# Kernel tuning notes

Measured on AMD Instinct MI355X. Metric: run time of the kernel, lower is better.

## Reference

```python
import jax, jax.numpy as jnp
import numpy as np

BATCH = 2
TIME_N = 196
SPACE_F = 8
D_MODEL = 768
N_HEADS = 12
D_STATE = 16
DT_RANK = 48  # ceil(768/16)
D_CONV = 4
SEQ = 1 + TIME_N * SPACE_F


def _ln(x, w, b, eps=1e-5):
    m = x.mean(-1, keepdims=True)
    v = ((x - m) ** 2).mean(-1, keepdims=True)
    return (x - m) * jax.lax.rsqrt(v + eps) * w + b


def _silu(x):
    return x * jax.nn.sigmoid(x)


def _causal_conv(x, w, b):
    # x: (B, L, d); depthwise causal conv1d, kernel D_CONV, padding left
    L = x.shape[1]
    xp = jnp.pad(x, ((0, 0), (D_CONV - 1, 0), (0, 0)))
    return sum(xp[:, k:k + L, :] * w[:, k] for k in range(D_CONV)) + b


def _ssm(u, delta, A, Bm, C, Dp):
    # u, delta: (B,L,d); A: (d,N); Bm, C: (B,L,N)
    dA = jnp.exp(delta[..., None] * A)                    # (B,L,d,N)
    dBu = (delta * u)[..., None] * Bm[:, :, None, :]      # (B,L,d,N)
    B, L, d, N = dA.shape

    def step(h, inp):
        a, bu = inp
        h = a * h + bu
        return h, h

    _, hs = jax.lax.scan(step, jnp.zeros((B, d, N), dA.dtype),
                         (dA.transpose(1, 0, 2, 3), dBu.transpose(1, 0, 2, 3)))
    return jnp.einsum('lbdn,bln->bld', hs, C) + u * Dp


def _mamba_dir(xp, z, conv_w, conv_b, xproj_w, dt_w, dt_b, A_log, Dp, flip):
    if flip:
        xp = xp[:, ::-1]
        z = z[:, ::-1]
    xc = _silu(_causal_conv(xp, conv_w, conv_b))
    x_dbl = xc @ xproj_w.T
    dt = x_dbl[..., :DT_RANK]
    Bm = x_dbl[..., DT_RANK:DT_RANK + D_STATE]
    C = x_dbl[..., DT_RANK + D_STATE:]
    delta = jax.nn.softplus(dt @ dt_w.T + dt_b)
    y = _ssm(xc, delta, -jnp.exp(A_log), Bm, C, Dp) * _silu(z)
    if flip:
        y = y[:, ::-1]
    return y


def _mamba(x, in_w, cw, cb, xw, dw, db, Al, Dp, cwb, cbb, xwb, dwb, dbb, Alb, Dpb, out_w):
    # bimamba v2: forward scan + backward (flipped) scan, summed, then out_proj
    xz = x @ in_w.T
    xp, z = jnp.split(xz, 2, axis=-1)
    y = (_mamba_dir(xp, z, cw, cb, xw, dw, db, Al, Dp, False)
         + _mamba_dir(xp, z, cwb, cbb, xwb, dwb, dbb, Alb, Dpb, True))
    return y @ out_w.T


def _mha(x, in_w, in_b, out_w, out_b):
    # torch nn.MultiheadAttention default (batch_first=False):
    # x is (L, N, E); attention runs over dim 0 (L), dim 1 (N) is batch.
    L, N, E = x.shape
    hd = E // N_HEADS
    qkv = x @ in_w.T + in_b
    q, k, v = jnp.split(qkv, 3, axis=-1)
    q = q.reshape(L, N, N_HEADS, hd)
    k = k.reshape(L, N, N_HEADS, hd)
    v = v.reshape(L, N, N_HEADS, hd)
    scores = jnp.einsum('lnhk,mnhk->nhlm', q, k) / jnp.sqrt(jnp.asarray(hd, x.dtype))
    o = jnp.einsum('nhlm,mnhk->lnhk', jax.nn.softmax(scores, axis=-1), v)
    return o.reshape(L, N, E) @ out_w.T + out_b


def _forward(x, norm1_w, norm1_b, norm2_w, norm2_b, norm3_w, norm3_b,
             attn_in_w, attn_in_b, attn_out_w, attn_out_b,
             m_in_w, m_conv_w, m_conv_b, m_xproj_w, m_dt_w, m_dt_b, m_Alog, m_D,
             m_conv_wb, m_conv_bb, m_xproj_wb, m_dt_wb, m_dt_bb, m_Alog_b, m_D_b,
             m_out_w, fc1_w, fc1_b, fc2_w, fc2_b, time_n, space_f):
    b, _, d = x.shape
    init_cls = x[:, :1]
    res_x = x
    # 'b (n t) d -> (b n) t d'
    xt = x[:, 1:].reshape(b, time_n, space_f, d).reshape(b * time_n, space_f, d)
    time_out = _mamba(_ln(xt, norm3_w, norm3_b), m_in_w, m_conv_w, m_conv_b,
                      m_xproj_w, m_dt_w, m_dt_b, m_Alog, m_D,
                      m_conv_wb, m_conv_bb, m_xproj_wb, m_dt_wb, m_dt_bb,
                      m_Alog_b, m_D_b, m_out_w)
    time_res = (xt + time_out).reshape(b, time_n, space_f, d)
    # cls repeat: 'b t d -> (b t) 1 d'
    cls = jnp.repeat(init_cls, space_f, axis=1).reshape(b * space_f, 1, d)
    # 'b (n t) d -> (b t) n d'
    xs = time_res.transpose(0, 2, 1, 3).reshape(b * space_f, time_n, d)
    xs = jnp.concatenate([cls, xs], axis=1)  # (b*t, n+1, d)
    space_out = _mha(_ln(xs, norm1_w, norm1_b), attn_in_w, attn_in_b, attn_out_w, attn_out_b)
    cls_tok = space_out[:, 0].reshape(b, space_f, d).mean(1, keepdims=True)
    # '(b t) n d -> b (n t) d'
    sp = space_out[:, 1:].reshape(b, space_f, time_n, d).transpose(0, 2, 1, 3).reshape(b, time_n * space_f, d)
    x = res_x + jnp.concatenate([cls_tok, sp], axis=1)
    h = _ln(x, norm2_w, norm2_b)
    h = jax.nn.gelu(h @ fc1_w.T + fc1_b, approximate=False) @ fc2_w.T + fc2_b
    return x + h


def setup_inputs():
    ks = iter(jax.random.split(jax.random.key(0), 64))

    def nrm(shape, s=0.02):
        return jax.random.normal(next(ks), shape, dtype=jnp.float32) * s

    d = D_MODEL
    Alog = jnp.log(jnp.tile(jnp.arange(1, D_STATE + 1, dtype=jnp.float32), (d, 1)))
    return dict(
        x=jax.random.normal(next(ks), (BATCH, SEQ, d), dtype=jnp.float32),
        norm1_w=jnp.ones((d,), jnp.float32), norm1_b=jnp.zeros((d,), jnp.float32),
        norm2_w=jnp.ones((d,), jnp.float32), norm2_b=jnp.zeros((d,), jnp.float32),
        norm3_w=jnp.ones((d,), jnp.float32), norm3_b=jnp.zeros((d,), jnp.float32),
        attn_in_w=nrm((3 * d, d)), attn_in_b=nrm((3 * d,)),
        attn_out_w=nrm((d, d)), attn_out_b=nrm((d,)),
        m_in_w=nrm((2 * d, d)),
        m_conv_w=nrm((d, D_CONV), 0.2), m_conv_b=nrm((d,), 0.1),
        m_xproj_w=nrm((DT_RANK + 2 * D_STATE, d)),
        m_dt_w=nrm((d, DT_RANK), 0.1), m_dt_b=nrm((d,), 0.5),
        m_Alog=Alog, m_D=jnp.ones((d,), jnp.float32),
        m_conv_wb=nrm((d, D_CONV), 0.2), m_conv_bb=nrm((d,), 0.1),
        m_xproj_wb=nrm((DT_RANK + 2 * D_STATE, d)),
        m_dt_wb=nrm((d, DT_RANK), 0.1), m_dt_bb=nrm((d,), 0.5),
        m_Alog_b=Alog, m_D_b=jnp.ones((d,), jnp.float32),
        m_out_w=nrm((d, d)),
        fc1_w=nrm((4 * d, d)), fc1_b=nrm((4 * d,), 0.01),
        fc2_w=nrm((d, 4 * d)), fc2_b=nrm((d,), 0.01),
        time_n=TIME_N, space_f=SPACE_F,
    )


def reference(x, norm1_w, norm1_b, norm2_w, norm2_b, norm3_w, norm3_b,
              attn_in_w, attn_in_b, attn_out_w, attn_out_b,
              m_in_w, m_conv_w, m_conv_b, m_xproj_w, m_dt_w, m_dt_b, m_Alog, m_D,
              m_conv_wb, m_conv_bb, m_xproj_wb, m_dt_wb, m_dt_bb, m_Alog_b, m_D_b,
              m_out_w, fc1_w, fc1_b, fc2_w, fc2_b, time_n, space_f):
    return _forward(x, norm1_w, norm1_b, norm2_w, norm2_b, norm3_w, norm3_b,
                    attn_in_w, attn_in_b, attn_out_w, attn_out_b,
                    m_in_w, m_conv_w, m_conv_b, m_xproj_w, m_dt_w, m_dt_b, m_Alog, m_D,
                    m_conv_wb, m_conv_bb, m_xproj_wb, m_dt_wb, m_dt_bb, m_Alog_b, m_D_b,
                    m_out_w, fc1_w, fc1_b, fc2_w, fc2_b, time_n, space_f)
```

## Files before the change

kernel.cpp:

```cpp
#include <hip/hip_runtime.h>
#include <hip/hip_bf16.h>
#include <math.h>

#define DM 768
#define NBATCH 2
#define TIMEN 196
#define SPACEF 8
#define SEQL 1569
#define NSTATE 16
#define MT 3136
#define NSEQ 392
#define AT 3152
#define XTOK 3138

typedef __attribute__((ext_vector_type(8))) short s16x8;
typedef __attribute__((ext_vector_type(4))) float f32x4;
typedef __hip_bfloat16 bf16;

__device__ __forceinline__ float silu_fast(float x){ return __fdividef(x, 1.0f + __expf(-x)); }
__device__ __forceinline__ float geluf(float x){ return 0.5f*x*(1.0f + erff(x*0.70710678118654752f)); }
__device__ __forceinline__ float softplusf(float x){ return (x > 20.0f) ? x : log1pf(expf(x)); }
__device__ __forceinline__ int imin(int a, int b){ return a < b ? a : b; }

#define GLD_LDS16(g, l) __builtin_amdgcn_global_load_lds( \
    (const __attribute__((address_space(1))) void*)(g), \
    (__attribute__((address_space(3))) void*)(l), 16, 0, 0)

template<int N, int K, int Np, int Kp>
__device__ __forceinline__ void cvt_seg(const float* __restrict__ src, bf16* __restrict__ dst){
  const int total = Np * Kp;
  int base = blockIdx.x * 1024 + threadIdx.x;
  #pragma unroll
  for (int e = 0; e < 4; e++){
    int idx = base + e * 256;
    if (idx < total){
      int n = idx / Kp, k = idx % Kp;
      float v = (n < N && k < K) ? src[n * K + k] : 0.0f;
      dst[idx] = __float2bfloat16(v);
    }
  }
}

__global__ __launch_bounds__(256) void cvtw_kernel(
    const float* s0, const float* s1, const float* s2, const float* s3,
    const float* s4, const float* s5, const float* s6, const float* s7,
    const float* s8, const float* s9, bf16* w)
{
  switch (blockIdx.y) {
    case 0: cvt_seg<1536,768,1536,768>(s0, w + 0);        break;
    case 1: cvt_seg<  80,768, 128,768>(s1, w + 1179648);  break;
    case 2: cvt_seg<  80,768, 128,768>(s2, w + 1277952);  break;
    case 3: cvt_seg< 768, 48, 768, 64>(s3, w + 1376256);  break;
    case 4: cvt_seg< 768, 48, 768, 64>(s4, w + 1425408);  break;
    case 5: cvt_seg< 768,768, 768,768>(s5, w + 1474560);  break;
    case 6: cvt_seg<2304,768,2304,768>(s6, w + 2064384);  break;
    case 7: cvt_seg< 768,768, 768,768>(s7, w + 3833856);  break;
    case 8: cvt_seg<3072,768,3072,768>(s8, w + 4423680);  break;
    default:cvt_seg< 768,3072,768,3072>(s9, w + 6782976); break;
  }
}

__device__ __forceinline__ float block_sum256(float v, float* sm){
  #pragma unroll
  for (int o = 32; o > 0; o >>= 1) v += __shfl_down(v, o);
  __syncthreads();
  if ((threadIdx.x & 63) == 0) sm[threadIdx.x >> 6] = v;
  __syncthreads();
  return sm[0] + sm[1] + sm[2] + sm[3];
}

__global__ __launch_bounds__(256) void ln_kernel(
    const float* __restrict__ src0, const float* __restrict__ src1,
    const float* __restrict__ w, const float* __restrict__ b,
    bf16* __restrict__ out, int mode)
{
  __shared__ float sm[4];
  int tok = blockIdx.x;
  const float* src;
  if (mode == 0) {
    src = src0 + (size_t)tok * DM;
  } else if (mode == 1) {
    int bi = tok / (TIMEN*SPACEF), r = tok % (TIMEN*SPACEF);
    src = src0 + ((size_t)bi * SEQL + 1 + r) * DM;
  } else {
    int sidx = tok / 197, p = tok % 197;
    if (p == 0) src = src0 + (size_t)(sidx >> 3) * SEQL * DM;
    else { int bi = sidx >> 3, f = sidx & 7, t = p - 1;
           src = src1 + (size_t)((bi*TIMEN + t)*SPACEF + f) * DM; }
  }
  int tid = threadIdx.x;
  float xr[3];
  #pragma unroll
  for (int i = 0; i < 3; i++) xr[i] = src[tid + i*256];
  float mean = block_sum256(xr[0]+xr[1]+xr[2], sm) * (1.0f/768.0f);
  float v0 = xr[0]-mean, v1 = xr[1]-mean, v2 = xr[2]-mean;
  float var = block_sum256(v0*v0 + v1*v1 + v2*v2, sm) * (1.0f/768.0f);
  float rstd = rsqrtf(var + 1e-5f);
  bf16* o = out + (size_t)tok * DM;
  #pragma unroll
  for (int i = 0; i < 3; i++){ int c = tid + i*256;
    o[c] = __float2bfloat16((xr[i]-mean)*rstd*w[c] + b[c]); }
}

template<int BM, int BN>
__global__ __launch_bounds__(256) void mgemm(
    const bf16* __restrict__ A, int lda,
    const bf16* __restrict__ W0, const bf16* __restrict__ W1, int ldw,
    const float* __restrict__ bias0, const float* __restrict__ bias1,
    const float* __restrict__ resid,
    void* __restrict__ Cout, int M, int mhalf, int N, int ldc, int KP,
    int act, int resmode, int outbf16, int skw)
{
  constexpr int AG = BM/64;
  constexpr int BG = BN/64;
  constexpr int WM = BM/2, WN = BN/2, MI = WM/16, NJ = WN/16;
  __shared__ bf16 As[2][BM*32];
  __shared__ bf16 Bs[2][BN*32];
  int tid = threadIdx.x;
  int wave = tid >> 6, lane = tid & 63;

  int nwg = gridDim.x * gridDim.y;
  int bid = blockIdx.y * gridDim.x + blockIdx.x;
  int q = nwg >> 3, r = nwg & 7;
  int xcd = bid & 7, lidx = bid >> 3;
  int wg = (xcd < r ? xcd*(q+1) : r*(q+1) + (xcd-r)*q) + lidx;
  int m0 = (wg / gridDim.x) * BM, n0 = (wg % gridDim.x) * BN;

  int wr = wave >> 1, wc = wave & 1;

  int koff = blockIdx.z * KP;
  const bf16* Ak = A + koff;
  const bf16* Wt = ((m0 < mhalf) ? W0 : W1) + koff;
  const float* bias = (m0 < mhalf) ? bias0 : bias1;

  f32x4 acc[MI][NJ];
  #pragma unroll
  for (int i = 0; i < MI; i++)
    #pragma unroll
    for (int j = 0; j < NJ; j++) acc[i][j] = (f32x4){0.f,0.f,0.f,0.f};

  int sr4 = lane >> 2, sc0 = (lane & 3) * 8;
  int lr16 = lane & 15, ks = (lane >> 4) * 8;

  auto stage = [&](int buf, int k0){
    #pragma unroll
    for (int g = 0; g < AG; g++){
      int rr = wave*(16*AG) + g*16;
      const bf16* ga = Ak + (size_t)imin(m0 + rr + sr4, M-1)*lda + k0 + sc0;
      GLD_LDS16(ga, &As[buf][rr*32]);
    }
    #pragma unroll
    for (int g = 0; g < BG; g++){
      int rr = wave*(16*BG) + g*16;
      const bf16* gb = Wt + (size_t)(n0 + rr + sr4)*ldw + k0 + sc0;
      GLD_LDS16(gb, &Bs[buf][rr*32]);
    }
  };

  auto compute = [&](int buf){
    s16x8 afr[MI], bfr[NJ];
    #pragma unroll
    for (int i = 0; i < MI; i++) afr[i] = *(const s16x8*)&As[buf][(wr*WM + i*16 + lr16)*32 + ks];
    #pragma unroll
    for (int j = 0; j < NJ; j++) bfr[j] = *(const s16x8*)&Bs[buf][(wc*WN + j*16 + lr16)*32 + ks];
    #pragma unroll
    for (int i = 0; i < MI; i++)
      #pragma unroll
      for (int j = 0; j < NJ; j++)
        acc[i][j] = __builtin_amdgcn_mfma_f32_16x16x32_bf16(afr[i], bfr[j], acc[i][j], 0, 0, 0);
  };

  stage(0, 0);
  __syncthreads();
  int cur = 0;
  for (int k0 = 32; k0 < KP; k0 += 32){
    stage(cur ^ 1, k0);
    compute(cur);
    __syncthreads();
    cur ^= 1;
  }
  compute(cur);

  #pragma unroll
  for (int i = 0; i < MI; i++){
    int rowb = m0 + wr*WM + i*16 + (lane >> 4)*4;
    #pragma unroll
    for (int j = 0; j < NJ; j++){
      int col = n0 + wc*WN + j*16 + lr16;
      if (col >= N) continue;
      float bv = bias ? bias[col] : 0.0f;
      #pragma unroll
      for (int r2 = 0; r2 < 4; r2++){
        int row = rowb + r2;
        if (row >= M) continue;
        float v = acc[i][j][r2];
        if (skw > 1){
          ((float*)Cout)[((size_t)(blockIdx.z*M) + row)*ldc + col] = v;
          continue;
        }
        v += bv;
        if (act == 1) v = geluf(v);
        else if (act == 2) v = softplusf(v);
        if (resmode == 1) v += resid[(size_t)row*ldc + col];
        else if (resmode == 2){
          int bi = row / (TIMEN*SPACEF), rr = row % (TIMEN*SPACEF);
          v += resid[((size_t)bi*SEQL + 1 + rr)*DM + col];
        }
        if (outbf16) ((bf16*)Cout)[(size_t)row*ldc + col] = __float2bfloat16(v);
        else         ((float*)Cout)[(size_t)row*ldc + col] = v;
      }
    }
  }
}

__global__ __launch_bounds__(256) void redk(
    const float* __restrict__ part, const float* __restrict__ bias,
    const float* __restrict__ resid, float* __restrict__ out,
    int M, int sk, int resmode)
{
  int i = blockIdx.x*256 + threadIdx.x;
  if (i*4 >= M*768) return;
  int row = i / 192;
  int c4 = (i - row*192) * 4;
  size_t base = (size_t)row*768 + c4;
  float4 v = *(const float4*)(part + base);
  for (int z = 1; z < sk; z++){
    float4 p = *(const float4*)(part + (size_t)z*M*768 + base);
    v.x += p.x; v.y += p.y; v.z += p.z; v.w += p.w;
  }
  if (bias){
    float4 b = *(const float4*)(bias + c4);
    v.x += b.x; v.y += b.y; v.z += b.z; v.w += b.w;
  }
  if (resmode == 1){
    float4 r = *(const float4*)(resid + base);
    v.x += r.x; v.y += r.y; v.z += r.z; v.w += r.w;
  } else if (resmode == 2){
    int bi = row / (TIMEN*SPACEF), rr = row % (TIMEN*SPACEF);
    float4 r = *(const float4*)(resid + ((size_t)bi*SEQL + 1 + rr)*DM + c4);
    v.x += r.x; v.y += r.y; v.z += r.z; v.w += r.w;
  }
  *(float4*)(out + base) = v;
}

__global__ __launch_bounds__(256) void conv_kernel(
    const float* __restrict__ xz,
    const float* __restrict__ wf, const float* __restrict__ bf,
    const float* __restrict__ wb, const float* __restrict__ bb,
    bf16* __restrict__ xcf, bf16* __restrict__ xcb)
{
  int g = blockIdx.x*256 + threadIdx.x;
  if (g >= NSEQ*DM) return;
  int s = g / DM, d = g % DM;
  float xr[8];
  #pragma unroll
  for (int j = 0; j < 8; j++) xr[j] = xz[(size_t)(s*8 + j)*1536 + d];
  float wfv[4], wbv[4];
  #pragma unroll
  for (int k = 0; k < 4; k++){ wfv[k] = wf[d*4+k]; wbv[k] = wb[d*4+k]; }
  float bfv = bf[d], bbv = bb[d];
  #pragma unroll
  for (int l = 0; l < 8; l++) {
    float af = bfv, ab = bbv;
    #pragma unroll
    for (int k = 0; k < 4; k++) {
      if (l + k >= 3) {
        af += wfv[k] * xr[l + k - 3];
        ab += wbv[k] * xr[10 - l - k];
      }
    }
    xcf[(size_t)(s*8 + l)*DM + d] = __float2bfloat16(silu_fast(af));
    xcb[(size_t)(s*8 + l)*DM + d] = __float2bfloat16(silu_fast(ab));
  }
}

__global__ __launch_bounds__(256) void ssm_kernel(
    const float* __restrict__ xz,
    const bf16* __restrict__ xcf, const bf16* __restrict__ xcb,
    const bf16* __restrict__ dblf, const bf16* __restrict__ dblb,
    const bf16* __restrict__ dlf, const bf16* __restrict__ dlb,
    const float* __restrict__ Alogf, const float* __restrict__ Df,
    const float* __restrict__ Alogb, const float* __restrict__ Db,
    bf16* __restrict__ y)
{
  int s = blockIdx.y;
  int d = blockIdx.x*256 + threadIdx.x;
  int tid = threadIdx.x;
  __shared__ float sBC[2][8][32];
  #pragma unroll
  for (int i = 0; i < 2; i++){
    int idx = tid + i*256;
    int dir = idx >> 8, r = idx & 255, l = r >> 5, j = r & 31;
    const bf16* p = dir ? dblb : dblf;
    sBC[dir][l][j] = __bfloat162float(p[(size_t)(s*8 + l)*80 + 48 + j]);
  }
  float Af[NSTATE], Ab[NSTATE];
  #pragma unroll
  for (int n = 0; n < NSTATE; n++) {
    Af[n] = -__expf(Alogf[d*NSTATE + n]);
    Ab[n] = -__expf(Alogb[d*NSTATE + n]);
  }
  float Dfv = Df[d], Dbv = Db[d];
  __syncthreads();

  float hf[NSTATE] = {}, hb[NSTATE] = {};
  float yf[8], yb[8];
  #pragma unroll
  for (int l = 0; l < 8; l++) {
    int t = s*8 + l;
    float delf = __bfloat162float(dlf[(size_t)t*DM + d]);
    float uf   = __bfloat162float(xcf[(size_t)t*DM + d]);
    float duf  = delf * uf;
    float accf = 0.0f;
    #pragma unroll
    for (int n = 0; n < NSTATE; n++) {
      hf[n] = __expf(delf*Af[n])*hf[n] + duf*sBC[0][l][n];
      accf += hf[n]*sBC[0][l][16+n];
    }
    yf[l] = accf + uf*Dfv;
    float delb = __bfloat162float(dlb[(size_t)t*DM + d]);
    float ub   = __bfloat162float(xcb[(size_t)t*DM + d]);
    float dub  = delb * ub;
    float accb = 0.0f;
    #pragma unroll
    for (int n = 0; n < NSTATE; n++) {
      hb[n] = __expf(delb*Ab[n])*hb[n] + dub*sBC[1][l][n];
      accb += hb[n]*sBC[1][l][16+n];
    }
    yb[7-l] = accb + ub*Dbv;
  }
  #pragma unroll
  for (int l = 0; l < 8; l++) {
    int t = s*8 + l;
    float zv = xz[(size_t)t*1536 + DM + d];
    y[(size_t)t*DM + d] = __float2bfloat16((yf[l] + yb[l]) * silu_fast(zv));
  }
}

__global__ __launch_bounds__(256) void attn_kernel(
    const bf16* __restrict__ qkv, bf16* __restrict__ ao)
{
  int n = blockIdx.x / 12, h = blockIdx.x % 12;
  __shared__ float qs[16][65], ks[16][65], vs[16][65], ps[16][17];
  int tid = threadIdx.x;
  for (int e = tid; e < 1024; e += 256) {
    int l = e >> 6, c = e & 63;
    size_t row = ((size_t)l*197 + n)*2304 + h*64 + c;
    qs[l][c] = __bfloat162float(qkv[row]);
    ks[l][c] = __bfloat162float(qkv[row + 768]);
    vs[l][c] = __bfloat162float(qkv[row + 1536]);
  }
  __syncthreads();
  int l = tid >> 4, m = tid & 15;
  float sc = 0.0f;
  #pragma unroll
  for (int c = 0; c < 64; c++) sc += qs[l][c]*ks[m][c];
  sc *= 0.125f;
  float mx = sc;
  #pragma unroll
  for (int o = 8; o > 0; o >>= 1) mx = fmaxf(mx, __shfl_xor(mx, o, 16));
  float p = __expf(sc - mx);
  float smv = p;
  #pragma unroll
  for (int o = 8; o > 0; o >>= 1) smv += __shfl_xor(smv, o, 16);
  ps[l][m] = __fdividef(p, smv);
  __syncthreads();
  for (int e = tid; e < 1024; e += 256) {
    int ll = e >> 6, c = e & 63;
    float acc = 0.0f;
    #pragma unroll
    for (int mm = 0; mm < 16; mm++) acc += ps[ll][mm]*vs[mm][c];
    ao[((size_t)ll*197 + n)*768 + h*64 + c] = __float2bfloat16(acc);
  }
}

__global__ __launch_bounds__(256) void scatter_kernel(
    const float* __restrict__ x, const float* __restrict__ so,
    float* __restrict__ xnew)
{
  int idx = blockIdx.x*256 + threadIdx.x;
  if (idx >= NBATCH*SEQL*DM) return;
  int bi = idx / (SEQL*DM);
  int rem = idx % (SEQL*DM);
  int row = rem / DM, d = rem % DM;
  float v;
  if (row == 0) {
    float acc = 0.0f;
    #pragma unroll
    for (int f = 0; f < SPACEF; f++)
      acc += so[((size_t)(bi*SPACEF + f)*197)*DM + d];
    v = x[idx] + acc * 0.125f;
  } else {
    int t = (row - 1) >> 3, f = (row - 1) & 7;
    v = x[idx] + so[((size_t)(bi*SPACEF + f)*197 + 1 + t)*DM + d];
  }
  xnew[idx] = v;
}

extern "C" void kernel_launch(void* const* d_in, const int* in_sizes, int n_in,
                              void* d_out, int out_size, void* d_ws, size_t ws_size,
                              hipStream_t stream) {
  const float* x        = (const float*)d_in[0];
  const float* norm1_w  = (const float*)d_in[1];
  const float* norm1_b  = (const float*)d_in[2];
  const float* norm2_w  = (const float*)d_in[3];
  const float* norm2_b  = (const float*)d_in[4];
  const float* norm3_w  = (const float*)d_in[5];
  const float* norm3_b  = (const float*)d_in[6];
  const float* attn_in_w  = (const float*)d_in[7];
  const float* attn_in_b  = (const float*)d_in[8];
  const float* attn_out_w = (const float*)d_in[9];
  const float* attn_out_b = (const float*)d_in[10];
  const float* m_in_w   = (const float*)d_in[11];
  const float* m_conv_w = (const float*)d_in[12];
  const float* m_conv_b = (const float*)d_in[13];
  const float* m_xproj_w= (const float*)d_in[14];
  const float* m_dt_w   = (const float*)d_in[15];
  const float* m_dt_b   = (const float*)d_in[16];
  const float* m_Alog   = (const float*)d_in[17];
  const float* m_D      = (const float*)d_in[18];
  const float* m_conv_wb= (const float*)d_in[19];
  const float* m_conv_bb= (const float*)d_in[20];
  const float* m_xproj_wb=(const float*)d_in[21];
  const float* m_dt_wb  = (const float*)d_in[22];
  const float* m_dt_bb  = (const float*)d_in[23];
  const float* m_Alog_b = (const float*)d_in[24];
  const float* m_D_b    = (const float*)d_in[25];
  const float* m_out_w  = (const float*)d_in[26];
  const float* fc1_w    = (const float*)d_in[27];
  const float* fc1_b    = (const float*)d_in[28];
  const float* fc2_w    = (const float*)d_in[29];
  const float* fc2_b    = (const float*)d_in[30];

  char* wsb = (char*)d_ws;
  bf16*  wpool  = (bf16*)(wsb + 0);
  bf16*  ln3    = (bf16*)(wsb + 18284544);
  float* xz     = (float*)(wsb + 23101440);
  bf16*  xcf    = (bf16*)(wsb + 42369024);
  bf16*  xcb    = (bf16*)(wsb + 47185920);
  bf16*  dblf   = (bf16*)(wsb + 52002816);
  bf16*  dblb   = (bf16*)(wsb + 52504576);
  bf16*  dlf    = (bf16*)(wsb + 53006336);
  bf16*  dlb    = (bf16*)(wsb + 57823232);
  bf16*  y      = ln3;
  float* tres   = (float*)(wsb + 62640128);
  float* part1  = (float*)(wsb + 23101440);
  bf16*  xsln   = (bf16*)(wsb + 23101440);
  float* so     = (float*)(wsb + 27942912);
  bf16*  qkv    = (bf16*)(wsb + 42369024);
  bf16*  ao     = (bf16*)(wsb + 18284544);
  float* part2  = (float*)(wsb + 42369024);
  float* xnew   = tres;
  bf16*  ln2o   = (bf16*)(wsb + 23101440);
  bf16*  h1     = (bf16*)(wsb + 42369024);
  float* part3  = (float*)(wsb + 18284544);

  bf16* w_in  = wpool + 0;
  bf16* w_xpf = wpool + 1179648;
  bf16* w_xpb = wpool + 1277952;
  bf16* w_dtf = wpool + 1376256;
  bf16* w_dtb = wpool + 1425408;
  bf16* w_out = wpool + 1474560;
  bf16* w_qkv = wpool + 2064384;
  bf16* w_ao  = wpool + 3833856;
  bf16* w_fc1 = wpool + 4423680;
  bf16* w_fc2 = wpool + 6782976;

  const int BIGM = 1 << 30;

  cvtw_kernel<<<dim3(2304, 10), 256, 0, stream>>>(
      m_in_w, m_xproj_w, m_xproj_wb, m_dt_w, m_dt_wb, m_out_w,
      attn_in_w, attn_out_w, fc1_w, fc2_w, wpool);

  ln_kernel<<<MT, 256, 0, stream>>>(x, nullptr, norm3_w, norm3_b, ln3, 1);
  mgemm<64,64><<<dim3(24, 49), 256, 0, stream>>>(ln3, DM, w_in, w_in, DM,
      nullptr, nullptr, nullptr, xz, MT, BIGM, 1536, 1536, DM, 0, 0, 0, 1);
  conv_kernel<<<(NSEQ*DM + 255)/256, 256, 0, stream>>>(
      xz, m_conv_w, m_conv_b, m_conv_wb, m_conv_bb, xcf, xcb);
  mgemm<64,64><<<dim3(2, 98), 256, 0, stream>>>(xcf, DM, w_xpf, w_xpb, DM,
      nullptr, nullptr, nullptr, dblf, 2*MT, MT, 80, 80, DM, 0, 0, 1, 1);
  mgemm<64,64><<<dim3(12, 98), 256, 0, stream>>>(dblf, 80, w_dtf, w_dtb, 64,
      m_dt_b, m_dt_bb, nullptr, dlf, 2*MT, MT, DM, DM, 64, 2, 0, 1, 1);
  ssm_kernel<<<dim3(3, NSEQ), 256, 0, stream>>>(
      xz, xcf, xcb, dblf, dblb, dlf, dlb, m_Alog, m_D, m_Alog_b, m_D_b, y);
  mgemm<64,64><<<dim3(12, 49, 2), 256, 0, stream>>>(y, DM, w_out, w_out, DM,
      nullptr, nullptr, nullptr, part1, MT, BIGM, DM, DM, 384, 0, 0, 0, 2);
  redk<<<2352, 256, 0, stream>>>(part1, nullptr, x, tres, MT, 2, 2);

  ln_kernel<<<AT, 256, 0, stream>>>(x, tres, norm1_w, norm1_b, xsln, 2);
  mgemm<64,64><<<dim3(36, 50), 256, 0, stream>>>(xsln, DM, w_qkv, w_qkv, DM,
      attn_in_b, attn_in_b, nullptr, qkv, AT, BIGM, 2304, 2304, DM, 0, 0, 1, 1);
  attn_kernel<<<197*12, 256, 0, stream>>>(qkv, ao);
  mgemm<64,64><<<dim3(12, 50, 2), 256, 0, stream>>>(ao, DM, w_ao, w_ao, DM,
      nullptr, nullptr, nullptr, part2, AT, BIGM, DM, DM, 384, 0, 0, 0, 2);
  redk<<<2364, 256, 0, stream>>>(part2, attn_out_b, nullptr, so, AT, 2, 0);
  scatter_kernel<<<(NBATCH*SEQL*DM + 255)/256, 256, 0, stream>>>(x, so, xnew);

  ln_kernel<<<XTOK, 256, 0, stream>>>(xnew, nullptr, norm2_w, norm2_b, ln2o, 0);
  mgemm<64,64><<<dim3(48, 50), 256, 0, stream>>>(ln2o, DM, w_fc1, w_fc1, DM,
      fc1_b, fc1_b, nullptr, h1, XTOK, BIGM, 3072, 3072, DM, 1, 0, 1, 1);
  mgemm<64,64><<<dim3(12, 50, 2), 256, 0, stream>>>(h1, 3072, w_fc2, w_fc2, 3072,
      nullptr, nullptr, nullptr, part3, XTOK, BIGM, DM, DM, 1536, 0, 0, 0, 2);
  redk<<<2354, 256, 0, stream>>>(part3, fc2_b, xnew, (float*)d_out, XTOK, 2, 1);
}
```

Measured before the change: 315.6 us.

## Double GEMM K-tile to 64 with XOR-swizzled LDS; use fast GELU/softplus approximations

The mfma GEMM now stages 64-wide K tiles instead of 32, halving the number of barrier-separated iterations. It also applies an XOR swizzle to the LDS layout so fragment reads avoid bank conflicts. Separately, erf-based GELU is replaced by the tanh approximation built on fast exp, and softplus uses fast log/exp. This trades more LDS per block (possibly lower occupancy) and some numeric accuracy in GELU for fewer syncs and cheaper transcendental math. It also assumes KP is a multiple of 64.

```diff
diff --git a/kernel.cpp b/kernel.cpp
--- a/kernel.cpp
+++ b/kernel.cpp
@@ -18,8 +18,17 @@
 typedef __hip_bfloat16 bf16;
 
 __device__ __forceinline__ float silu_fast(float x){ return __fdividef(x, 1.0f + __expf(-x)); }
-__device__ __forceinline__ float geluf(float x){ return 0.5f*x*(1.0f + erff(x*0.70710678118654752f)); }
-__device__ __forceinline__ float softplusf(float x){ return (x > 20.0f) ? x : log1pf(expf(x)); }
+__device__ __forceinline__ float geluf(float x){
+  float y = 0.7978845608f * (x + 0.044715f*x*x*x);
+  float ay = fabsf(y);
+  float e = __expf(-2.0f*ay);
+  float t = __fdividef(1.0f - e, 1.0f + e);
+  t = copysignf(t, y);
+  return 0.5f*x*(1.0f + t);
+}
+__device__ __forceinline__ float softplusf(float x){
+  return (x > 20.0f) ? x : __logf(1.0f + __expf(x));
+}
 __device__ __forceinline__ int imin(int a, int b){ return a < b ? a : b; }
 
 #define GLD_LDS16(g, l) __builtin_amdgcn_global_load_lds( \
@@ -111,11 +120,9 @@
     void* __restrict__ Cout, int M, int mhalf, int N, int ldc, int KP,
     int act, int resmode, int outbf16, int skw)
 {
-  constexpr int AG = BM/64;
-  constexpr int BG = BN/64;
   constexpr int WM = BM/2, WN = BN/2, MI = WM/16, NJ = WN/16;
-  __shared__ bf16 As[2][BM*32];
-  __shared__ bf16 Bs[2][BN*32];
+  __shared__ bf16 As[2][BM*64];
+  __shared__ bf16 Bs[2][BN*64];
   int tid = threadIdx.x;
   int wave = tid >> 6, lane = tid & 63;
 
@@ -139,41 +146,50 @@
     #pragma unroll
     for (int j = 0; j < NJ; j++) acc[i][j] = (f32x4){0.f,0.f,0.f,0.f};
 
-  int sr4 = lane >> 2, sc0 = (lane & 3) * 8;
+  int sr8 = lane >> 3;
+  int scs = (((lane & 7) ^ sr8) * 8);
   int lr16 = lane & 15, ks = (lane >> 4) * 8;
+  int swz = (lr16 & 7) << 3;
 
   auto stage = [&](int buf, int k0){
     #pragma unroll
-    for (int g = 0; g < AG; g++){
-      int rr = wave*(16*AG) + g*16;
-      const bf16* ga = Ak + (size_t)imin(m0 + rr + sr4, M-1)*lda + k0 + sc0;
-      GLD_LDS16(ga, &As[buf][rr*32]);
-    }
-    #pragma unroll
-    for (int g = 0; g < BG; g++){
-      int rr = wave*(16*BG) + g*16;
-      const bf16* gb = Wt + (size_t)(n0 + rr + sr4)*ldw + k0 + sc0;
-      GLD_LDS16(gb, &Bs[buf][rr*32]);
+    for (int g = 0; g < BM/32; g++){
+      int rr = wave*(BM/4) + g*8;
+      const bf16* ga = Ak + (size_t)imin(m0 + rr + sr8, M-1)*lda + k0 + scs;
+      GLD_LDS16(ga, &As[buf][rr*64]);
+    }
+    #pragma unroll
+    for (int g = 0; g < BN/32; g++){
+      int rr = wave*(BN/4) + g*8;
+      const bf16* gb = Wt + (size_t)(n0 + rr + sr8)*ldw + k0 + scs;
+      GLD_LDS16(gb, &Bs[buf][rr*64]);
     }
   };
 
   auto compute = [&](int buf){
-    s16x8 afr[MI], bfr[NJ];
-    #pragma unroll
-    for (int i = 0; i < MI; i++) afr[i] = *(const s16x8*)&As[buf][(wr*WM + i*16 + lr16)*32 + ks];
-    #pragma unroll
-    for (int j = 0; j < NJ; j++) bfr[j] = *(const s16x8*)&Bs[buf][(wc*WN + j*16 + lr16)*32 + ks];
-    #pragma unroll
-    for (int i = 0; i < MI; i++)
+    s16x8 afr[2][MI], bfr[2][NJ];
+    #pragma unroll
+    for (int kk = 0; kk < 2; kk++){
+      #pragma unroll
+      for (int i = 0; i < MI; i++)
+        afr[kk][i] = *(const s16x8*)&As[buf][(wr*WM + i*16 + lr16)*64 + ((kk*32 + ks) ^ swz)];
       #pragma unroll
       for (int j = 0; j < NJ; j++)
-        acc[i][j] = __builtin_amdgcn_mfma_f32_16x16x32_bf16(afr[i], bfr[j], acc[i][j], 0, 0, 0);
+        bfr[kk][j] = *(const s16x8*)&Bs[buf][(wc*WN + j*16 + lr16)*64 + ((kk*32 + ks) ^ swz)];
+    }
+    #pragma unroll
+    for (int kk = 0; kk < 2; kk++)
+      #pragma unroll
+      for (int i = 0; i < MI; i++)
+        #pragma unroll
+        for (int j = 0; j < NJ; j++)
+          acc[i][j] = __builtin_amdgcn_mfma_f32_16x16x32_bf16(afr[kk][i], bfr[kk][j], acc[i][j], 0, 0, 0);
   };
 
   stage(0, 0);
   __syncthreads();
   int cur = 0;
-  for (int k0 = 32; k0 < KP; k0 += 32){
+  for (int k0 = 64; k0 < KP; k0 += 64){
     stage(cur ^ 1, k0);
     compute(cur);
     __syncthreads();
```

New measurement: 290.1 us. 1.09x faster.
